# Kernel tuning notes

Measured on AMD Instinct MI355X. Metric: run time of the kernel, lower is better.

Reference implementation:

```python
import jax, jax.numpy as jnp
import numpy as np

B, C, D, H, W = 2, 3, 4, 32, 32
N = D * H * W
REAL_SIZE = jnp.array([3.0, 25.0, 25.0], dtype=jnp.float32)
CUTOFFS = jnp.array([1.0, 0.75], dtype=jnp.float32)   # cutoff[c-1] for class c in {1,2}
SPLIT = [0.0, 3.0 + 1e-5]                             # split[-1] += 1e-5 as in __init__
S = len(SPLIT) - 1
NMS_ITERS = 32  # fixed-point iterations; greedy-NMS update is idempotent once converged


def setup_inputs() -> dict:
    key = jax.random.key(0)
    k1, k2, k3, k4 = jax.random.split(key, 4)
    return {
        "pred_clses": jax.random.normal(k1, (B, C, D, H, W), dtype=jnp.float32),
        "pred_boxes": jax.random.normal(k2, (B, 3, D, H, W), dtype=jnp.float32),
        "targ_clses": jax.random.randint(k3, (B, D, H, W), 0, C),
        "targ_boxes": jax.random.uniform(k4, (B, D, H, W, 3), dtype=jnp.float32),
    }


def _pdist2(a, b):
    # squared euclidean cdist without materializing [N,N,3]
    aa = (a * a).sum(-1)
    bb = (b * b).sum(-1)
    return jnp.maximum(aa[:, None] + bb[None, :] - 2.0 * (a @ b.T), 0.0)


def _grid():
    d, h, w = jnp.meshgrid(jnp.arange(D), jnp.arange(H), jnp.arange(W), indexing="ij")
    return jnp.stack([d, h, w], -1).reshape(N, 3).astype(jnp.float32)


def _confusion(pred_pos, conf, pred_arg, targ_pos, targ_cls, c, cutoff):
    # mask-based (fixed-shape, jit-safe) version of the per-(batch,class) loop body
    valid_p = pred_arg == c
    # self.sort: confidence-descending order (invalid points pushed to the end)
    order = jnp.argsort(-jnp.where(valid_p, conf, -jnp.inf))
    pos = pred_pos[order]      # [N,3] physical coords (already * real_size)
    valid = valid_p[order]
    c2 = cutoff * cutoff
    # triu conflict graph restricted to valid points; order fixed => shrinking
    # DIS[SELECT][:,SELECT] in the original == masking rows/cols by 'alive' here
    conflict = (_pdist2(pos, pos) < c2) & jnp.triu(jnp.ones((N, N), bool), 1) \
               & valid[:, None] & valid[None, :]

    def body(_, alive):
        Mf = (conflict & alive[:, None] & alive[None, :]).astype(jnp.float32)
        restrain = Mf.sum(0)
        restrain = restrain - (restrain != 0).astype(jnp.float32) @ Mf
        return alive & (restrain == 0)

    alive = jax.lax.fori_loop(0, NMS_ITERS, body, valid)  # NMS fixed point

    # match(): targets hit by any surviving prediction within cutoff
    valid_t = targ_cls == c
    matched = ((_pdist2(pos, targ_pos) < c2) & alive[:, None]).any(0)
    z_p, z_t = pos[:, 0], targ_pos[:, 0]
    rows = []
    for i in range(S):
        lo, hi = SPLIT[i], SPLIT[i + 1]
        lp = alive & (z_p >= lo) & (z_p < hi)
        lt = valid_t & (z_t >= lo) & (z_t < hi)
        tp = (lt & matched).sum()
        rows.append(jnp.stack([tp, lp.sum() - tp, lt.sum() - tp]))  # TP, FP, FN
    return jnp.stack(rows)  # [S,3]


def _forward(pred_clses, pred_boxes, targ_clses, targ_boxes):
    grid, dims = _grid(), jnp.array([D, H, W], jnp.float32)
    pc = pred_clses.transpose(0, 2, 3, 4, 1).reshape(B, N, C)
    conf, arg = pc.max(-1), pc.argmax(-1)
    pb = jax.nn.sigmoid(pred_boxes.transpose(0, 2, 3, 4, 1).reshape(B, N, 3))
    # boxncls2pos: (voxel index + in-cell offset) / grid dims -> [0,1]^3, then * real_size
    pred_pos = (grid + pb) / dims * REAL_SIZE
    targ_pos = (grid + targ_boxes.reshape(B, N, 3)) / dims * REAL_SIZE
    tcls = targ_clses.reshape(B, N)
    cs = jnp.arange(1, C)
    per_cls = jax.vmap(_confusion, in_axes=(None, None, None, None, None, 0, 0))
    per_b = jax.vmap(per_cls, in_axes=(0, 0, 0, 0, 0, None, None))
    return per_b(pred_pos, conf, arg, targ_pos, tcls, cs, CUTOFFS)  # [B, C-1, S, 3]


def reference(pred_clses, pred_boxes, targ_clses, targ_boxes):
    return _forward(pred_clses, pred_boxes, targ_clses, targ_boxes)
```

## Files before the change

kernel.cpp:

```cpp
#include <hip/hip_runtime.h>
#include <cstdint>
#include <cstddef>

typedef unsigned long long u64;
typedef unsigned int u32;
typedef unsigned short u16;

#define N_ 4096
#define KCAP_ 32
#define SENT_ 4096

__device__ __forceinline__ float sigf(float x) { return 1.0f / (1.0f + expf(-x)); }

#define ANY4B(arr, wa, wb) \
  ((int)((arr)[(wa) & 0xFFFFu] | (arr)[(wa) >> 16] | \
         (arr)[(wb) & 0xFFFFu] | (arr)[(wb) >> 16]))

template <int EXT>
__device__ __forceinline__ int build_preds(
    const float4* __restrict__ hp, float4 self, int d0, int hl, int wl, int n,
    float cut2, u16* __restrict__ rowp) {
  u32 okey = __float_as_uint(self.w);
  int cnt = 0;
  #pragma unroll
  for (int dd = -EXT; dd <= EXT; ++dd) {
    #pragma unroll
    for (int dh = -EXT; dh <= EXT; ++dh) {
      #pragma unroll
      for (int dw = -EXT; dw <= EXT; ++dw) {
        if (dd == 0 && dh == 0 && dw == 0) continue;
        if ((dd * dd == 4) + (dh * dh == 4) + (dw * dw == 4) > 1) continue;
        int d2 = d0 + dd;
        if ((u32)d2 >= 4u) continue;
        float4 pn = hp[d2 * 144 + (hl + dh) * 12 + (wl + dw)];
        float dx = pn.x - self.x, dy = pn.y - self.y, dz = pn.z - self.z;
        float dsq = dx * dx + dy * dy + dz * dz;
        u32 ok2 = __float_as_uint(pn.w);
        int n2 = n + (dd << 10) + (dh << 5) + dw;
        bool pred = (dsq < cut2) && (ok2 > okey || (ok2 == okey && n2 < n));
        if (pred) {
          if (cnt < KCAP_) rowp[cnt] = (u16)n2;
          cnt++;
        }
      }
    }
  }
  return cnt;
}

__global__ __launch_bounds__(256) void k_build(
    const float* __restrict__ pc, const float* __restrict__ pb,
    float4* __restrict__ posG, int* __restrict__ deg, u16* __restrict__ predL) {
  int blk = blockIdx.x;
  int pair = blk >> 4, tile = blk & 15;
  int b = pair >> 1, c = (pair & 1) + 1;
  int th0 = ((tile >> 2) << 3);
  int tw0 = ((tile & 3) << 3);
  __shared__ float4 hpos[576];
  const float* pcb = pc + (size_t)b * 3 * N_;
  const float* pbb = pb + (size_t)b * 3 * N_;
  for (int e = threadIdx.x; e < 576; e += 256) {
    int d = e / 144, rem = e - d * 144;
    int hh = rem / 12, ww = rem - hh * 12;
    int h = th0 + hh - 2, w = tw0 + ww - 2;
    float4 v; v.x = 1e9f; v.y = 1e9f; v.z = 1e9f; v.w = 0.f;
    if ((u32)h < 32u && (u32)w < 32u) {
      int n = (d << 10) | (h << 5) | w;
      float v0 = pcb[n], v1 = pcb[n + N_], v2 = pcb[n + 2 * N_];
      float cf = v0; int a = 0;
      if (v1 > cf) { cf = v1; a = 1; }
      if (v2 > cf) { cf = v2; a = 2; }
      if (a == c) {
        u32 o = __float_as_uint(cf);
        o ^= (o >> 31) ? 0xFFFFFFFFu : 0x80000000u;
        v.x = ((float)d + sigf(pbb[n])) * 0.75f;
        v.y = ((float)h + sigf(pbb[n + N_])) * 0.78125f;
        v.z = ((float)w + sigf(pbb[n + 2 * N_])) * 0.78125f;
        v.w = __uint_as_float(o);
      }
    }
    hpos[e] = v;
  }
  __syncthreads();
  int tid = threadIdx.x;
  int d0 = tid >> 6;
  int hl = ((tid >> 3) & 7) + 2;
  int wl = (tid & 7) + 2;
  int n = (d0 << 10) | ((th0 + hl - 2) << 5) | (tw0 + wl - 2);
  float4 self = hpos[d0 * 144 + hl * 12 + wl];
  posG[pair * N_ + n] = self;
  u16* rowp = predL + (((size_t)(pair * N_ + n)) << 5);
  int cnt = 0;
  if (self.x < 1e8f) {
    if (pair & 1) cnt = build_preds<1>(hpos, self, d0, hl, wl, n, 0.5625f, rowp);
    else          cnt = build_preds<2>(hpos, self, d0, hl, wl, n, 1.0f, rowp);
    if (cnt > KCAP_) cnt = KCAP_;
  }
  deg[pair * N_ + n] = cnt;
  int pad = (cnt + 3) & ~3;
  for (int s = cnt; s < pad; ++s) rowp[s] = (u16)SENT_;
}

__global__ __launch_bounds__(1024) void k_nms(
    const float4* __restrict__ posG, const int* __restrict__ deg,
    const u16* __restrict__ predL,
    float4* __restrict__ alivePosG, int* __restrict__ out) {
  int pair = blockIdx.x, tid = threadIdx.x;
  __shared__ unsigned char aliveB[4112];
  __shared__ unsigned char freeB[4112];
  __shared__ int flag[2], acnt;
  float4 pos[4]; int dg[4]; u32 pw[4][4]; bool al[4];
  #pragma unroll
  for (int q = 0; q < 4; ++q) {
    int r = tid + (q << 10);
    pos[q] = posG[pair * N_ + r];
    al[q] = (pos[q].x < 1e8f);
    dg[q] = deg[pair * N_ + r];
    uint4 t = *(const uint4*)(predL + (((size_t)(pair * N_ + r)) << 5));
    pw[q][0] = t.x; pw[q][1] = t.y; pw[q][2] = t.z; pw[q][3] = t.w;
    aliveB[r] = al[q];
    freeB[r] = 0;
  }
  if (tid < 16) { aliveB[4096 + tid] = 0; freeB[4096 + tid] = 0; }
  if (tid == 0) { flag[0] = 0; flag[1] = 0; acnt = 0; }
  __syncthreads();

  for (int iter = 0; iter < 32; ++iter) {
    if (tid == 0) flag[(iter + 1) & 1] = 0;
    #pragma unroll
    for (int q = 0; q < 4; ++q) {
      int r = tid + (q << 10);
      bool fr = al[q];
      if (al[q] && dg[q]) {
        int any = ANY4B(aliveB, pw[q][0], pw[q][1]);
        if (dg[q] > 4) any |= ANY4B(aliveB, pw[q][2], pw[q][3]);
        if (dg[q] > 8) {
          const u16* rowp = predL + (((size_t)(pair * N_ + r)) << 5);
          for (int k = 8; k < dg[q]; ++k) any |= aliveB[rowp[k]];
        }
        fr = (any == 0);
      }
      freeB[r] = fr;
    }
    __syncthreads();
    int lch = 0;
    #pragma unroll
    for (int q = 0; q < 4; ++q) {
      int r = tid + (q << 10);
      if (al[q] && dg[q]) {
        int any = ANY4B(freeB, pw[q][0], pw[q][1]);
        if (dg[q] > 4) any |= ANY4B(freeB, pw[q][2], pw[q][3]);
        if (dg[q] > 8) {
          const u16* rowp = predL + (((size_t)(pair * N_ + r)) << 5);
          for (int k = 8; k < dg[q]; ++k) any |= freeB[rowp[k]];
        }
        if (any) { al[q] = false; aliveB[r] = 0; lch = 1; }
      }
    }
    if (lch) flag[iter & 1] = 1;
    __syncthreads();
    if (!flag[iter & 1]) break;
  }

  float4 dead; dead.x = 1e9f; dead.y = 1e9f; dead.z = 1e9f; dead.w = 0.f;
  #pragma unroll
  for (int q = 0; q < 4; ++q) {
    int r = tid + (q << 10);
    alivePosG[pair * N_ + r] = al[q] ? pos[q] : dead;
    u64 ball = __ballot(al[q]);
    if ((tid & 63) == 0 && ball) atomicAdd(&acnt, __popcll(ball));
  }
  __syncthreads();
  if (tid == 0) {
    out[pair * 3 + 0] = 0;
    out[pair * 3 + 1] = acnt;
    out[pair * 3 + 2] = 0;
  }
}

template <int EXT>
__device__ __forceinline__ int match_ball(
    const float4* __restrict__ alive, int n, float tx, float ty, float tz,
    float cut2) {
  int d0 = n >> 10, h0 = (n >> 5) & 31, w0 = n & 31;
  int m = 0;
  #pragma unroll
  for (int dd = -EXT; dd <= EXT; ++dd) {
    #pragma unroll
    for (int dh = -EXT; dh <= EXT; ++dh) {
      #pragma unroll
      for (int dw = -EXT; dw <= EXT; ++dw) {
        if ((dd * dd == 4) + (dh * dh == 4) + (dw * dw == 4) > 1) continue;
        int d2i = d0 + dd, h2i = h0 + dh, w2i = w0 + dw;
        if ((u32)d2i < 4u && (u32)h2i < 32u && (u32)w2i < 32u) {
          int n2 = (d2i << 10) | (h2i << 5) | w2i;
          float4 p = alive[n2];
          float dx = p.x - tx, dy = p.y - ty, dz = p.z - tz;
          m |= (int)(dx * dx + dy * dy + dz * dz < cut2);
        }
      }
    }
  }
  return m;
}

__global__ __launch_bounds__(256) void k_match(
    const float4* __restrict__ alivePosG,
    const int* __restrict__ tcls, const float* __restrict__ tb,
    int* __restrict__ out) {
  int idx = blockIdx.x * 256 + threadIdx.x;
  int pair = idx >> 12, n = idx & (N_ - 1);
  int b = pair >> 1, c = (pair & 1) + 1;
  float cut2 = (pair & 1) ? 0.5625f : 1.0f;
  __shared__ int s_tp, s_t;
  if (threadIdx.x == 0) { s_tp = 0; s_t = 0; }
  __syncthreads();
  int isC = (tcls[b * N_ + n] == c) ? 1 : 0;
  float d = (float)(n >> 10), h = (float)((n >> 5) & 31), w = (float)(n & 31);
  const float* tbp = tb + ((size_t)b * N_ + n) * 3;
  float tx = (d + tbp[0]) * 0.75f;
  float ty = (h + tbp[1]) * 0.78125f;
  float tz = (w + tbp[2]) * 0.78125f;
  const float4* alive = alivePosG + (size_t)pair * N_;
  int m;
  if (pair & 1) m = match_ball<1>(alive, n, tx, ty, tz, cut2);
  else          m = match_ball<2>(alive, n, tx, ty, tz, cut2);
  m &= isC;
  atomicAdd(&s_tp, m);
  atomicAdd(&s_t, isC);
  __syncthreads();
  if (threadIdx.x == 0) {
    atomicAdd(&out[pair * 3 + 0], s_tp);
    atomicAdd(&out[pair * 3 + 1], -s_tp);
    atomicAdd(&out[pair * 3 + 2], s_t - s_tp);
  }
}

extern "C" void kernel_launch(void* const* d_in, const int* in_sizes, int n_in,
                              void* d_out, int out_size, void* d_ws, size_t ws_size,
                              hipStream_t stream) {
  (void)in_sizes; (void)n_in; (void)out_size; (void)ws_size;
  const float* pc = (const float*)d_in[0];
  const float* pb = (const float*)d_in[1];
  const int*   tc = (const int*)d_in[2];
  const float* tb = (const float*)d_in[3];
  int* out = (int*)d_out;

  char* ws = (char*)d_ws;
  size_t off = 0;
  auto alloc = [&](size_t bytes) -> void* {
    void* p = ws + off;
    off += (bytes + 255) & ~(size_t)255;
    return p;
  };
  float4* posG      = (float4*)alloc((size_t)4 * N_ * 16);
  int*    deg       = (int*)alloc((size_t)4 * N_ * 4);
  u16*    predL     = (u16*)alloc((size_t)4 * N_ * KCAP_ * 2);
  float4* alivePosG = (float4*)alloc((size_t)4 * N_ * 16);

  k_build<<<64, 256, 0, stream>>>(pc, pb, posG, deg, predL);
  k_nms<<<4, 1024, 0, stream>>>(posG, deg, predL, alivePosG, out);
  k_match<<<64, 256, 0, stream>>>(alivePosG, tc, tb, out);
}
```

Measured before the change: 103.8 us.

## Replace predecessor polling in NMS with successor-push counters

The NMS graph now stores successor lists plus a predecessor count instead of predecessor lists. Each iteration re-scanned every predecessor's alive/free byte; now newly dead points atomically decrement their successors' counters, and newly free points clear their successors' alive bytes. Work is spread across iterations as events happen rather than repeated polling. k_nms also marks dead points in posG in place, dropping the separate alivePosG buffer. This trades gathered byte reads for shared-memory atomics and global reads of successor rows each time something changes.

```diff
diff --git a/kernel.cpp b/kernel.cpp
--- a/kernel.cpp
+++ b/kernel.cpp
@@ -7,21 +7,16 @@
 typedef unsigned short u16;
 
 #define N_ 4096
-#define KCAP_ 32
-#define SENT_ 4096
+#define SROW_ 48
 
 __device__ __forceinline__ float sigf(float x) { return 1.0f / (1.0f + expf(-x)); }
 
-#define ANY4B(arr, wa, wb) \
-  ((int)((arr)[(wa) & 0xFFFFu] | (arr)[(wa) >> 16] | \
-         (arr)[(wb) & 0xFFFFu] | (arr)[(wb) >> 16]))
-
 template <int EXT>
-__device__ __forceinline__ int build_preds(
+__device__ __forceinline__ int build_adj(
     const float4* __restrict__ hp, float4 self, int d0, int hl, int wl, int n,
     float cut2, u16* __restrict__ rowp) {
   u32 okey = __float_as_uint(self.w);
-  int cnt = 0;
+  int pcnt = 0, scnt = 0;
   #pragma unroll
   for (int dd = -EXT; dd <= EXT; ++dd) {
     #pragma unroll
@@ -35,22 +30,27 @@
         float4 pn = hp[d2 * 144 + (hl + dh) * 12 + (wl + dw)];
         float dx = pn.x - self.x, dy = pn.y - self.y, dz = pn.z - self.z;
         float dsq = dx * dx + dy * dy + dz * dz;
-        u32 ok2 = __float_as_uint(pn.w);
-        int n2 = n + (dd << 10) + (dh << 5) + dw;
-        bool pred = (dsq < cut2) && (ok2 > okey || (ok2 == okey && n2 < n));
-        if (pred) {
-          if (cnt < KCAP_) rowp[cnt] = (u16)n2;
-          cnt++;
+        if (dsq < cut2) {
+          u32 ok2 = __float_as_uint(pn.w);
+          int n2 = n + (dd << 10) + (dh << 5) + dw;
+          bool earlier = (ok2 > okey) || (ok2 == okey && n2 < n);
+          if (earlier) {
+            pcnt++;
+          } else {
+            if (scnt < SROW_ - 1) rowp[1 + scnt] = (u16)n2;
+            scnt++;
+          }
         }
       }
     }
   }
-  return cnt;
+  rowp[0] = (u16)(scnt < SROW_ ? scnt : SROW_ - 1);
+  return pcnt;
 }
 
 __global__ __launch_bounds__(256) void k_build(
     const float* __restrict__ pc, const float* __restrict__ pb,
-    float4* __restrict__ posG, int* __restrict__ deg, u16* __restrict__ predL) {
+    float4* __restrict__ posG, int* __restrict__ pdeg, u16* __restrict__ succL) {
   int blk = blockIdx.x;
   int pair = blk >> 4, tile = blk & 15;
   int b = pair >> 1, c = (pair & 1) + 1;
@@ -88,86 +88,73 @@
   int wl = (tid & 7) + 2;
   int n = (d0 << 10) | ((th0 + hl - 2) << 5) | (tw0 + wl - 2);
   float4 self = hpos[d0 * 144 + hl * 12 + wl];
-  posG[pair * N_ + n] = self;
-  u16* rowp = predL + (((size_t)(pair * N_ + n)) << 5);
-  int cnt = 0;
+  int row = pair * N_ + n;
+  posG[row] = self;
+  int pd = -1;
   if (self.x < 1e8f) {
-    if (pair & 1) cnt = build_preds<1>(hpos, self, d0, hl, wl, n, 0.5625f, rowp);
-    else          cnt = build_preds<2>(hpos, self, d0, hl, wl, n, 1.0f, rowp);
-    if (cnt > KCAP_) cnt = KCAP_;
-  }
-  deg[pair * N_ + n] = cnt;
-  int pad = (cnt + 3) & ~3;
-  for (int s = cnt; s < pad; ++s) rowp[s] = (u16)SENT_;
+    u16* rowp = succL + (size_t)row * SROW_;
+    if (pair & 1) pd = build_adj<1>(hpos, self, d0, hl, wl, n, 0.5625f, rowp);
+    else          pd = build_adj<2>(hpos, self, d0, hl, wl, n, 1.0f, rowp);
+  }
+  pdeg[row] = pd;
 }
 
 __global__ __launch_bounds__(1024) void k_nms(
-    const float4* __restrict__ posG, const int* __restrict__ deg,
-    const u16* __restrict__ predL,
-    float4* __restrict__ alivePosG, int* __restrict__ out) {
+    const int* __restrict__ pdeg, const u16* __restrict__ succL,
+    float4* __restrict__ posG, int* __restrict__ out) {
   int pair = blockIdx.x, tid = threadIdx.x;
-  __shared__ unsigned char aliveB[4112];
-  __shared__ unsigned char freeB[4112];
+  __shared__ unsigned char aliveB[4096];
+  __shared__ int cntA[4096];
   __shared__ int flag[2], acnt;
-  float4 pos[4]; int dg[4]; u32 pw[4][4]; bool al[4];
+  bool al[4], fre[4], wasC[4];
   #pragma unroll
   for (int q = 0; q < 4; ++q) {
     int r = tid + (q << 10);
-    pos[q] = posG[pair * N_ + r];
-    al[q] = (pos[q].x < 1e8f);
-    dg[q] = deg[pair * N_ + r];
-    uint4 t = *(const uint4*)(predL + (((size_t)(pair * N_ + r)) << 5));
-    pw[q][0] = t.x; pw[q][1] = t.y; pw[q][2] = t.z; pw[q][3] = t.w;
-    aliveB[r] = al[q];
-    freeB[r] = 0;
-  }
-  if (tid < 16) { aliveB[4096 + tid] = 0; freeB[4096 + tid] = 0; }
+    int pd = pdeg[(pair << 12) + r];
+    al[q] = (pd >= 0); fre[q] = false; wasC[q] = (pd >= 0);
+    aliveB[r] = al[q] ? 1 : 0;
+    cntA[r] = pd > 0 ? pd : 0;
+  }
   if (tid == 0) { flag[0] = 0; flag[1] = 0; acnt = 0; }
   __syncthreads();
 
   for (int iter = 0; iter < 32; ++iter) {
-    if (tid == 0) flag[(iter + 1) & 1] = 0;
     #pragma unroll
     for (int q = 0; q < 4; ++q) {
       int r = tid + (q << 10);
-      bool fr = al[q];
-      if (al[q] && dg[q]) {
-        int any = ANY4B(aliveB, pw[q][0], pw[q][1]);
-        if (dg[q] > 4) any |= ANY4B(aliveB, pw[q][2], pw[q][3]);
-        if (dg[q] > 8) {
-          const u16* rowp = predL + (((size_t)(pair * N_ + r)) << 5);
-          for (int k = 8; k < dg[q]; ++k) any |= aliveB[rowp[k]];
+      if (al[q] && !fre[q]) {
+        if (!aliveB[r]) {
+          al[q] = false;
+          const u16* rp = succL + (size_t)((pair << 12) + r) * SROW_;
+          int sc = rp[0];
+          for (int k = 1; k <= sc; ++k) atomicSub(&cntA[rp[k]], 1);
         }
-        fr = (any == 0);
-      }
-      freeB[r] = fr;
+      }
     }
     __syncthreads();
     int lch = 0;
     #pragma unroll
     for (int q = 0; q < 4; ++q) {
       int r = tid + (q << 10);
-      if (al[q] && dg[q]) {
-        int any = ANY4B(freeB, pw[q][0], pw[q][1]);
-        if (dg[q] > 4) any |= ANY4B(freeB, pw[q][2], pw[q][3]);
-        if (dg[q] > 8) {
-          const u16* rowp = predL + (((size_t)(pair * N_ + r)) << 5);
-          for (int k = 8; k < dg[q]; ++k) any |= freeB[rowp[k]];
-        }
-        if (any) { al[q] = false; aliveB[r] = 0; lch = 1; }
-      }
-    }
+      if (al[q] && !fre[q] && cntA[r] == 0) {
+        fre[q] = true; lch = 1;
+        const u16* rp = succL + (size_t)((pair << 12) + r) * SROW_;
+        int sc = rp[0];
+        for (int k = 1; k <= sc; ++k) aliveB[rp[k]] = 0;
+      }
+    }
+    if (tid == 0) flag[(iter + 1) & 1] = 0;
     if (lch) flag[iter & 1] = 1;
     __syncthreads();
     if (!flag[iter & 1]) break;
   }
 
-  float4 dead; dead.x = 1e9f; dead.y = 1e9f; dead.z = 1e9f; dead.w = 0.f;
   #pragma unroll
   for (int q = 0; q < 4; ++q) {
     int r = tid + (q << 10);
-    alivePosG[pair * N_ + r] = al[q] ? pos[q] : dead;
-    u64 ball = __ballot(al[q]);
+    int a = aliveB[r];
+    if (!a && wasC[q]) posG[(pair << 12) + r].x = 1e9f;
+    u64 ball = __ballot(a != 0);
     if ((tid & 63) == 0 && ball) atomicAdd(&acnt, __popcll(ball));
   }
   __syncthreads();
@@ -205,7 +192,7 @@
 }
 
 __global__ __launch_bounds__(256) void k_match(
-    const float4* __restrict__ alivePosG,
+    const float4* __restrict__ posG,
     const int* __restrict__ tcls, const float* __restrict__ tb,
     int* __restrict__ out) {
   int idx = blockIdx.x * 256 + threadIdx.x;
@@ -221,7 +208,7 @@
   float tx = (d + tbp[0]) * 0.75f;
   float ty = (h + tbp[1]) * 0.78125f;
   float tz = (w + tbp[2]) * 0.78125f;
-  const float4* alive = alivePosG + (size_t)pair * N_;
+  const float4* alive = posG + (size_t)pair * N_;
   int m;
   if (pair & 1) m = match_ball<1>(alive, n, tx, ty, tz, cut2);
   else          m = match_ball<2>(alive, n, tx, ty, tz, cut2);
@@ -253,12 +240,11 @@
     off += (bytes + 255) & ~(size_t)255;
     return p;
   };
-  float4* posG      = (float4*)alloc((size_t)4 * N_ * 16);
-  int*    deg       = (int*)alloc((size_t)4 * N_ * 4);
-  u16*    predL     = (u16*)alloc((size_t)4 * N_ * KCAP_ * 2);
-  float4* alivePosG = (float4*)alloc((size_t)4 * N_ * 16);
-
-  k_build<<<64, 256, 0, stream>>>(pc, pb, posG, deg, predL);
-  k_nms<<<4, 1024, 0, stream>>>(posG, deg, predL, alivePosG, out);
-  k_match<<<64, 256, 0, stream>>>(alivePosG, tc, tb, out);
-}
+  float4* posG  = (float4*)alloc((size_t)4 * N_ * 16);
+  int*    pdeg  = (int*)alloc((size_t)4 * N_ * 4);
+  u16*    succL = (u16*)alloc((size_t)4 * N_ * SROW_ * 2);
+
+  k_build<<<64, 256, 0, stream>>>(pc, pb, posG, pdeg, succL);
+  k_nms<<<4, 1024, 0, stream>>>(pdeg, succL, posG, out);
+  k_match<<<64, 256, 0, stream>>>(posG, tc, tb, out);
+}
```

Result: no change. 103.6 us (-0.2%).
